# Performance work log

Hardware: AMD Instinct MI355X
Metric: run time of the kernel (lower is better)

The kernel has to match this reference:

```python
import jax, jax.numpy as jnp
import numpy as np

B = 16384      # batch
F = 26         # onehot fields
E = 32         # embedding_dim
L = 50         # multihot bag length
V = 1000000    # num_embeddings
CT = 13        # continuous features
D0, D1, D2, D3 = 909, 512, 256, 1
LEAKY = 0.01


def _leaky(x):
    return jnp.where(x >= 0, x, LEAKY * x)


def setup_inputs() -> dict:
    key = jax.random.key(0)
    ks = jax.random.split(key, 16)
    inp = {
        "onehot_i": jax.random.randint(ks[0], (B, F), 0, V),
        "onehot_x": jax.random.uniform(ks[1], (B, F), dtype=jnp.float32),
        "multihot_i1": jax.random.randint(ks[2], (B, L), 0, V),
        "multihot_x1": jax.random.uniform(ks[3], (B, L), dtype=jnp.float32),
        "multihot_i2": jax.random.randint(ks[4], (B, L), 0, V),
        "multihot_x2": jax.random.uniform(ks[5], (B, L), dtype=jnp.float32),
        "ctns": jax.random.normal(ks[6], (B, CT), dtype=jnp.float32),
        # learned parameters
        "wide_table": jax.random.normal(ks[7], (V, 1), dtype=jnp.float32) * 0.02,
        "deep_table": jax.random.normal(ks[8], (V, E), dtype=jnp.float32) * 0.02,
        "w2": jax.random.normal(ks[9], (D1, D0), dtype=jnp.float32) * (1.0 / np.sqrt(D0)),
        "b2": jnp.zeros((D1,), dtype=jnp.float32),
        "w3": jax.random.normal(ks[10], (D2, D1), dtype=jnp.float32) * (1.0 / np.sqrt(D1)),
        "b3": jnp.zeros((D2,), dtype=jnp.float32),
        "w4": jax.random.normal(ks[11], (D3, D2), dtype=jnp.float32) * (1.0 / np.sqrt(D2)),
        "b4": jnp.zeros((D3,), dtype=jnp.float32),
    }
    return inp


def reference(onehot_i, onehot_x, multihot_i1, multihot_x1, multihot_i2,
              multihot_x2, ctns, wide_table, deep_table, w2, b2, w3, b3, w4, b4):
    # ---- wide part ----
    # Original broadcasts the [B,F,1] wide embedding against x repeated E times,
    # then sums over all columns. That equals E * sum_f(w[idx]*x).
    wide_sum = (wide_table[onehot_i, 0] * onehot_x).sum(axis=1)          # [B]
    wide_sum = wide_sum + (wide_table[multihot_i1, 0] * multihot_x1).sum(axis=1)
    wide_sum = wide_sum + (wide_table[multihot_i2, 0] * multihot_x2).sum(axis=1)
    wide_out = E * wide_sum                                              # [B]

    # ---- deep part: gather, scale by field weight, pool multihot bags ----
    d_one = (deep_table[onehot_i] * onehot_x[:, :, None]).reshape(B, F * E)   # [B, F*E]
    d_m1 = (deep_table[multihot_i1] * multihot_x1[:, :, None]).sum(axis=1)    # [B, E]
    d_m2 = (deep_table[multihot_i2] * multihot_x2[:, :, None]).sum(axis=1)    # [B, E]
    x = jnp.concatenate([d_one, d_m1, d_m2, ctns], axis=1)                    # [B, D0]

    # dropout p=0.0 (deterministic reference)
    x = _leaky(x @ w2.T + b2)
    x = _leaky(x @ w3.T + b3)
    x = (x @ w4.T + b4).squeeze(-1)                                           # [B]
    return jax.nn.sigmoid(x + wide_out)
```

## Files before the change

### kernel.cpp

```cpp
#include <hip/hip_runtime.h>
#include <hip/hip_bf16.h>
#include <math.h>

#define B_   16384
#define F_   26
#define E_   32
#define L_   50
#define CT_  13
#define D0_  909
#define D0P  928
#define D1_  512
#define D2_  256

typedef __bf16 bf16x8 __attribute__((ext_vector_type(8)));
typedef float f32x4 __attribute__((ext_vector_type(4)));

__device__ inline float bf2f(unsigned short u) {
    union { unsigned int i; float f; } v; v.i = ((unsigned int)u) << 16; return v.f;
}
__device__ inline unsigned short f2b(float f) {
    union { __hip_bfloat16 h; unsigned short u; } v;
    v.h = __float2bfloat16(f);
    return v.u;
}

__device__ inline void gld_lds16(const void* g, void* l) {
    __builtin_amdgcn_global_load_lds(
        (const __attribute__((address_space(1))) unsigned int*)g,
        (__attribute__((address_space(3))) unsigned int*)l, 16, 0, 0);
}

#define W2N (D1_ * D0P)
#define W3N (D2_ * D1_)
__global__ __launch_bounds__(256) void cvt_weights(
    const float* __restrict__ w2, const float* __restrict__ w3,
    __hip_bfloat16* __restrict__ o2, __hip_bfloat16* __restrict__ o3)
{
    int i = blockIdx.x * 256 + threadIdx.x;
    if (i < W2N) {
        int r = i / D0P, c = i - r * D0P;
        float v = (c < D0_) ? w2[r * D0_ + c] : 0.f;
        o2[i] = __float2bfloat16(v);
    } else {
        int j = i - W2N;
        if (j < W3N) o3[j] = __float2bfloat16(w3[j]);
    }
}

__global__ __launch_bounds__(256) void embed_kernel(
    const int* __restrict__ oi, const float* __restrict__ ox,
    const int* __restrict__ i1, const float* __restrict__ x1,
    const int* __restrict__ i2, const float* __restrict__ x2,
    const float* __restrict__ ct, const float* __restrict__ wtab,
    const float* __restrict__ dtab,
    __hip_bfloat16* __restrict__ x0, float* __restrict__ wide)
{
    const int s    = blockIdx.x * 4 + (threadIdx.x >> 6);
    const int lane = threadIdx.x & 63;
    const int g    = lane >> 3;
    const int l    = lane & 7;
    __hip_bfloat16* xrow = x0 + (size_t)s * D0P;
    const float4* dt4 = (const float4*)dtab;

#pragma unroll
    for (int f0 = 0; f0 < 32; f0 += 8) {
        int f = f0 + g;
        if (f < F_) {
            int   idx = oi[s * F_ + f];
            float xv  = ox[s * F_ + f];
            float4 v  = dt4[(size_t)idx * 8 + l];
            ushort4 o;
            o.x = f2b(v.x * xv); o.y = f2b(v.y * xv);
            o.z = f2b(v.z * xv); o.w = f2b(v.w * xv);
            *(ushort4*)(xrow + f * E_ + l * 4) = o;
        }
    }

    float4 a1 = {0.f, 0.f, 0.f, 0.f}, a2 = {0.f, 0.f, 0.f, 0.f};
#pragma unroll
    for (int j0 = 0; j0 < 56; j0 += 8) {
        int j = j0 + g;
        if (j < L_) {
            int   k1 = i1[s * L_ + j];  float xv1 = x1[s * L_ + j];
            int   k2 = i2[s * L_ + j];  float xv2 = x2[s * L_ + j];
            float4 v1 = dt4[(size_t)k1 * 8 + l];
            float4 v2 = dt4[(size_t)k2 * 8 + l];
            a1.x = fmaf(v1.x, xv1, a1.x); a1.y = fmaf(v1.y, xv1, a1.y);
            a1.z = fmaf(v1.z, xv1, a1.z); a1.w = fmaf(v1.w, xv1, a1.w);
            a2.x = fmaf(v2.x, xv2, a2.x); a2.y = fmaf(v2.y, xv2, a2.y);
            a2.z = fmaf(v2.z, xv2, a2.z); a2.w = fmaf(v2.w, xv2, a2.w);
        }
    }
#pragma unroll
    for (int m = 8; m < 64; m <<= 1) {
        a1.x += __shfl_xor(a1.x, m); a1.y += __shfl_xor(a1.y, m);
        a1.z += __shfl_xor(a1.z, m); a1.w += __shfl_xor(a1.w, m);
        a2.x += __shfl_xor(a2.x, m); a2.y += __shfl_xor(a2.y, m);
        a2.z += __shfl_xor(a2.z, m); a2.w += __shfl_xor(a2.w, m);
    }
    if (g == 0) {
        ushort4 o;
        o.x = f2b(a1.x); o.y = f2b(a1.y); o.z = f2b(a1.z); o.w = f2b(a1.w);
        *(ushort4*)(xrow + F_ * E_ + l * 4) = o;
    }
    if (g == 1) {
        ushort4 o;
        o.x = f2b(a2.x); o.y = f2b(a2.y); o.z = f2b(a2.z); o.w = f2b(a2.w);
        *(ushort4*)(xrow + F_ * E_ + E_ + l * 4) = o;
    }
    if (lane < E_) {
        float v = (lane < CT_) ? ct[s * CT_ + lane] : 0.f;
        xrow[F_ * E_ + 2 * E_ + lane] = __float2bfloat16(v);
    }
    float acc = 0.f;
#pragma unroll
    for (int t = lane; t < F_ + 2 * L_; t += 64) {
        int idx; float xv;
        if (t < F_)            { idx = oi[s * F_ + t];            xv = ox[s * F_ + t]; }
        else if (t < F_ + L_)  { int j = t - F_;       idx = i1[s * L_ + j]; xv = x1[s * L_ + j]; }
        else                   { int j = t - F_ - L_;  idx = i2[s * L_ + j]; xv = x2[s * L_ + j]; }
        acc += wtab[idx] * xv;
    }
    for (int o = 32; o; o >>= 1) acc += __shfl_xor(acc, o);
    if (lane == 0) wide[s] = (float)E_ * acc;
}

template<int N, int K, bool ACT>
__global__ __launch_bounds__(256) void gemm_bias(
    const __hip_bfloat16* __restrict__ A,
    const __hip_bfloat16* __restrict__ W,
    const float* __restrict__ bias,
    __hip_bfloat16* __restrict__ C, int MBLKS)
{
    __shared__ __hip_bfloat16 As[128 * 32];
    __shared__ __hip_bfloat16 Bs[128 * 32];

    const int bm   = blockIdx.x % MBLKS;
    const int bn   = blockIdx.x / MBLKS;
    const int tid  = threadIdx.x;
    const int lane = tid & 63;
    const int w    = tid >> 6;
    const int wm   = w >> 1, wn = w & 1;

    f32x4 acc[4][4] = {};

    const int srow = lane >> 2;
    const int scol = (lane & 3) * 8;
    const __hip_bfloat16* Aw0 = A + ((size_t)bm * 128 + w * 32 + srow) * K + scol;
    const __hip_bfloat16* Aw1 = Aw0 + (size_t)16 * K;
    const __hip_bfloat16* Ww0 = W + ((size_t)bn * 128 + w * 32 + srow) * K + scol;
    const __hip_bfloat16* Ww1 = Ww0 + (size_t)16 * K;
    char* AsW = (char*)As + w * 2048;
    char* BsW = (char*)Bs + w * 2048;

    const int fr = lane & 15;
    const int kg = (lane >> 4) * 8;

    for (int k0 = 0; k0 < K; k0 += 32) {
        gld_lds16(Aw0 + k0, AsW);
        gld_lds16(Aw1 + k0, AsW + 1024);
        gld_lds16(Ww0 + k0, BsW);
        gld_lds16(Ww1 + k0, BsW + 1024);
        __syncthreads();

        bf16x8 af[4], bfv[4];
#pragma unroll
        for (int i = 0; i < 4; i++)
            af[i] = *(const bf16x8*)(As + (wm * 64 + i * 16 + fr) * 32 + kg);
#pragma unroll
        for (int i = 0; i < 4; i++)
            bfv[i] = *(const bf16x8*)(Bs + (wn * 64 + i * 16 + fr) * 32 + kg);
#pragma unroll
        for (int i = 0; i < 4; i++)
#pragma unroll
            for (int j = 0; j < 4; j++)
                acc[i][j] = __builtin_amdgcn_mfma_f32_16x16x32_bf16(af[i], bfv[j], acc[i][j], 0, 0, 0);
        __syncthreads();
    }

    float bv[4];
#pragma unroll
    for (int j = 0; j < 4; j++) bv[j] = bias[bn * 128 + wn * 64 + j * 16 + fr];
    const int crow0 = bm * 128 + wm * 64 + (lane >> 4) * 4;
    const int ccol0 = bn * 128 + wn * 64 + fr;
#pragma unroll
    for (int i = 0; i < 4; i++)
#pragma unroll
        for (int j = 0; j < 4; j++)
#pragma unroll
            for (int r = 0; r < 4; r++) {
                float v = acc[i][j][r] + bv[j];
                if (ACT) v = (v >= 0.f) ? v : 0.01f * v;
                C[(size_t)(crow0 + i * 16 + r) * N + ccol0 + j * 16] = __float2bfloat16(v);
            }
}

__global__ __launch_bounds__(256) void final_kernel(
    const __hip_bfloat16* __restrict__ h2, const float* __restrict__ w4,
    const float* __restrict__ b4, const float* __restrict__ wide,
    float* __restrict__ out)
{
    const int s    = blockIdx.x * 4 + (threadIdx.x >> 6);
    const int lane = threadIdx.x & 63;
    const unsigned short* hp = (const unsigned short*)(h2 + (size_t)s * D2_);
    ushort4 hv = *(const ushort4*)(hp + lane * 4);
    float4  wv = *(const float4*)(w4 + lane * 4);
    float acc = bf2f(hv.x) * wv.x + bf2f(hv.y) * wv.y + bf2f(hv.z) * wv.z + bf2f(hv.w) * wv.w;
    for (int o = 32; o; o >>= 1) acc += __shfl_xor(acc, o);
    if (lane == 0) {
        float x = acc + b4[0] + wide[s];
        out[s] = 1.f / (1.f + expf(-x));
    }
}

extern "C" void kernel_launch(void* const* d_in, const int* in_sizes, int n_in,
                              void* d_out, int out_size, void* d_ws, size_t ws_size,
                              hipStream_t stream) {
    const int*   oi  = (const int*)  d_in[0];
    const float* ox  = (const float*)d_in[1];
    const int*   i1  = (const int*)  d_in[2];
    const float* x1  = (const float*)d_in[3];
    const int*   i2  = (const int*)  d_in[4];
    const float* x2  = (const float*)d_in[5];
    const float* ct  = (const float*)d_in[6];
    const float* wt  = (const float*)d_in[7];
    const float* dt  = (const float*)d_in[8];
    const float* w2  = (const float*)d_in[9];
    const float* b2  = (const float*)d_in[10];
    const float* w3  = (const float*)d_in[11];
    const float* b3  = (const float*)d_in[12];
    const float* w4  = (const float*)d_in[13];
    const float* b4  = (const float*)d_in[14];
    float* out = (float*)d_out;

    char* ws = (char*)d_ws;
    __hip_bfloat16* x0b = (__hip_bfloat16*)(ws);
    __hip_bfloat16* h1b = (__hip_bfloat16*)(ws + 30408704);
    __hip_bfloat16* h2b = (__hip_bfloat16*)(ws + 47185920);
    float*          wid = (float*)         (ws + 55574528);
    __hip_bfloat16* w2b = (__hip_bfloat16*)(ws + 55640064);
    __hip_bfloat16* w3b = (__hip_bfloat16*)(ws + 56590336);

    cvt_weights<<<(W2N + W3N + 255) / 256, 256, 0, stream>>>(w2, w3, w2b, w3b);
    embed_kernel<<<4096, 256, 0, stream>>>(oi, ox, i1, x1, i2, x2, ct, wt, dt, x0b, wid);
    gemm_bias<D1_, D0P, true ><<<128 * (D1_ / 128), 256, 0, stream>>>(x0b, w2b, b2, h1b, 128);
    gemm_bias<D2_, D1_, true ><<<128 * (D2_ / 128), 256, 0, stream>>>(h1b, w3b, b3, h2b, 128);
    final_kernel<<<4096, 256, 0, stream>>>(h2b, w4, b4, wid, out);
}
```

Baseline: 126.5 us.

## Convert embedding table to bf16 before gathering and halve GEMM M-tile

Adds a kernel that converts the whole 1M x 32 fp32 deep table to bf16 in workspace on every call, then gathers from that bf16 copy, used only when the workspace is large enough. Separately, the GEMM tile is reduced from 128 to 64 rows so twice as many blocks launch. The table conversion streams 128MB in and writes 64MB per call to save on roughly 2M scattered 128B gathers, which is likely a net cost. The smaller M tile adds parallelism but reduces reuse of the weight tiles.

```diff
diff --git a/kernel.cpp b/kernel.cpp
--- a/kernel.cpp
+++ b/kernel.cpp
@@ -11,9 +11,12 @@
 #define D0P  928
 #define D1_  512
 #define D2_  256
+#define V_   1000000
+#define VE_  (V_ * E_)
 
 typedef __bf16 bf16x8 __attribute__((ext_vector_type(8)));
 typedef float f32x4 __attribute__((ext_vector_type(4)));
+typedef unsigned short u16x8 __attribute__((ext_vector_type(8)));
 
 __device__ inline float bf2f(unsigned short u) {
     union { unsigned int i; float f; } v; v.i = ((unsigned int)u) << 16; return v.f;
@@ -28,6 +31,19 @@
     __builtin_amdgcn_global_load_lds(
         (const __attribute__((address_space(1))) unsigned int*)g,
         (__attribute__((address_space(3))) unsigned int*)l, 16, 0, 0);
+}
+
+__global__ __launch_bounds__(256) void cvt_table(const float* __restrict__ dt,
+                                                 unsigned short* __restrict__ tb) {
+    size_t stride = (size_t)gridDim.x * 256 * 8;
+    for (size_t i = ((size_t)blockIdx.x * 256 + threadIdx.x) * 8; i < (size_t)VE_; i += stride) {
+        f32x4 a = __builtin_nontemporal_load((const f32x4*)(dt + i));
+        f32x4 b = __builtin_nontemporal_load((const f32x4*)(dt + i + 4));
+        u16x8 o;
+        o[0] = f2b(a.x); o[1] = f2b(a.y); o[2] = f2b(a.z); o[3] = f2b(a.w);
+        o[4] = f2b(b.x); o[5] = f2b(b.y); o[6] = f2b(b.z); o[7] = f2b(b.w);
+        *(u16x8*)(tb + i) = o;
+    }
 }
 
 #define W2N (D1_ * D0P)
@@ -47,7 +63,89 @@
     }
 }
 
-__global__ __launch_bounds__(256) void embed_kernel(
+__global__ __launch_bounds__(256) void embed_bf16(
+    const int* __restrict__ oi, const float* __restrict__ ox,
+    const int* __restrict__ i1, const float* __restrict__ x1,
+    const int* __restrict__ i2, const float* __restrict__ x2,
+    const float* __restrict__ ct, const float* __restrict__ wtab,
+    const unsigned short* __restrict__ tb,
+    __hip_bfloat16* __restrict__ x0, float* __restrict__ wide)
+{
+    const int s    = blockIdx.x * 4 + (threadIdx.x >> 6);
+    const int lane = threadIdx.x & 63;
+    const int g    = lane >> 2;
+    const int l    = lane & 3;
+    unsigned short* xrow = (unsigned short*)(x0 + (size_t)s * D0P);
+
+#pragma unroll
+    for (int f0 = 0; f0 < 32; f0 += 16) {
+        int f = f0 + g;
+        if (f < F_) {
+            int   idx = oi[s * F_ + f];
+            float xv  = ox[s * F_ + f];
+            u16x8 v = *(const u16x8*)(tb + (size_t)idx * E_ + l * 8);
+            u16x8 o;
+#pragma unroll
+            for (int e = 0; e < 8; e++) o[e] = f2b(bf2f(v[e]) * xv);
+            *(u16x8*)(xrow + f * E_ + l * 8) = o;
+        }
+    }
+
+    float a1[8] = {0.f,0.f,0.f,0.f,0.f,0.f,0.f,0.f};
+    float a2[8] = {0.f,0.f,0.f,0.f,0.f,0.f,0.f,0.f};
+#pragma unroll
+    for (int j0 = 0; j0 < 64; j0 += 16) {
+        int j = j0 + g;
+        if (j < L_) {
+            int   k1  = i1[s * L_ + j];  float xv1 = x1[s * L_ + j];
+            int   k2  = i2[s * L_ + j];  float xv2 = x2[s * L_ + j];
+            u16x8 v1 = *(const u16x8*)(tb + (size_t)k1 * E_ + l * 8);
+            u16x8 v2 = *(const u16x8*)(tb + (size_t)k2 * E_ + l * 8);
+#pragma unroll
+            for (int e = 0; e < 8; e++) {
+                a1[e] = fmaf(bf2f(v1[e]), xv1, a1[e]);
+                a2[e] = fmaf(bf2f(v2[e]), xv2, a2[e]);
+            }
+        }
+    }
+#pragma unroll
+    for (int m = 4; m < 64; m <<= 1) {
+#pragma unroll
+        for (int e = 0; e < 8; e++) {
+            a1[e] += __shfl_xor(a1[e], m);
+            a2[e] += __shfl_xor(a2[e], m);
+        }
+    }
+    if (g == 0) {
+        u16x8 o;
+#pragma unroll
+        for (int e = 0; e < 8; e++) o[e] = f2b(a1[e]);
+        *(u16x8*)(xrow + F_ * E_ + l * 8) = o;
+    }
+    if (g == 1) {
+        u16x8 o;
+#pragma unroll
+        for (int e = 0; e < 8; e++) o[e] = f2b(a2[e]);
+        *(u16x8*)(xrow + F_ * E_ + E_ + l * 8) = o;
+    }
+    if (lane < E_) {
+        float v = (lane < CT_) ? ct[s * CT_ + lane] : 0.f;
+        xrow[F_ * E_ + 2 * E_ + lane] = f2b(v);
+    }
+    float acc = 0.f;
+#pragma unroll
+    for (int t = lane; t < F_ + 2 * L_; t += 64) {
+        int idx; float xv;
+        if (t < F_)            { idx = oi[s * F_ + t];            xv = ox[s * F_ + t]; }
+        else if (t < F_ + L_)  { int j = t - F_;       idx = i1[s * L_ + j]; xv = x1[s * L_ + j]; }
+        else                   { int j = t - F_ - L_;  idx = i2[s * L_ + j]; xv = x2[s * L_ + j]; }
+        acc += wtab[idx] * xv;
+    }
+    for (int o = 32; o; o >>= 1) acc += __shfl_xor(acc, o);
+    if (lane == 0) wide[s] = (float)E_ * acc;
+}
+
+__global__ __launch_bounds__(256) void embed_fp32(
     const int* __restrict__ oi, const float* __restrict__ ox,
     const int* __restrict__ i1, const float* __restrict__ x1,
     const int* __restrict__ i2, const float* __restrict__ x2,
@@ -59,8 +157,8 @@
     const int lane = threadIdx.x & 63;
     const int g    = lane >> 3;
     const int l    = lane & 7;
-    __hip_bfloat16* xrow = x0 + (size_t)s * D0P;
-    const float4* dt4 = (const float4*)dtab;
+    unsigned short* xrow = (unsigned short*)(x0 + (size_t)s * D0P);
+    const f32x4* dt4 = (const f32x4*)dtab;
 
 #pragma unroll
     for (int f0 = 0; f0 < 32; f0 += 8) {
@@ -68,23 +166,22 @@
         if (f < F_) {
             int   idx = oi[s * F_ + f];
             float xv  = ox[s * F_ + f];
-            float4 v  = dt4[(size_t)idx * 8 + l];
+            f32x4 v   = dt4[(size_t)idx * 8 + l];
             ushort4 o;
             o.x = f2b(v.x * xv); o.y = f2b(v.y * xv);
             o.z = f2b(v.z * xv); o.w = f2b(v.w * xv);
             *(ushort4*)(xrow + f * E_ + l * 4) = o;
         }
     }
-
-    float4 a1 = {0.f, 0.f, 0.f, 0.f}, a2 = {0.f, 0.f, 0.f, 0.f};
+    f32x4 a1 = {0.f,0.f,0.f,0.f}, a2 = {0.f,0.f,0.f,0.f};
 #pragma unroll
     for (int j0 = 0; j0 < 56; j0 += 8) {
         int j = j0 + g;
         if (j < L_) {
-            int   k1 = i1[s * L_ + j];  float xv1 = x1[s * L_ + j];
-            int   k2 = i2[s * L_ + j];  float xv2 = x2[s * L_ + j];
-            float4 v1 = dt4[(size_t)k1 * 8 + l];
-            float4 v2 = dt4[(size_t)k2 * 8 + l];
+            int k1 = i1[s * L_ + j];  float xv1 = x1[s * L_ + j];
+            int k2 = i2[s * L_ + j];  float xv2 = x2[s * L_ + j];
+            f32x4 v1 = dt4[(size_t)k1 * 8 + l];
+            f32x4 v2 = dt4[(size_t)k2 * 8 + l];
             a1.x = fmaf(v1.x, xv1, a1.x); a1.y = fmaf(v1.y, xv1, a1.y);
             a1.z = fmaf(v1.z, xv1, a1.z); a1.w = fmaf(v1.w, xv1, a1.w);
             a2.x = fmaf(v2.x, xv2, a2.x); a2.y = fmaf(v2.y, xv2, a2.y);
@@ -99,18 +196,16 @@
         a2.z += __shfl_xor(a2.z, m); a2.w += __shfl_xor(a2.w, m);
     }
     if (g == 0) {
-        ushort4 o;
-        o.x = f2b(a1.x); o.y = f2b(a1.y); o.z = f2b(a1.z); o.w = f2b(a1.w);
+        ushort4 o; o.x = f2b(a1.x); o.y = f2b(a1.y); o.z = f2b(a1.z); o.w = f2b(a1.w);
         *(ushort4*)(xrow + F_ * E_ + l * 4) = o;
     }
     if (g == 1) {
-        ushort4 o;
-        o.x = f2b(a2.x); o.y = f2b(a2.y); o.z = f2b(a2.z); o.w = f2b(a2.w);
+        ushort4 o; o.x = f2b(a2.x); o.y = f2b(a2.y); o.z = f2b(a2.z); o.w = f2b(a2.w);
         *(ushort4*)(xrow + F_ * E_ + E_ + l * 4) = o;
     }
     if (lane < E_) {
         float v = (lane < CT_) ? ct[s * CT_ + lane] : 0.f;
-        xrow[F_ * E_ + 2 * E_ + lane] = __float2bfloat16(v);
+        xrow[F_ * E_ + 2 * E_ + lane] = f2b(v);
     }
     float acc = 0.f;
 #pragma unroll
@@ -132,7 +227,7 @@
     const float* __restrict__ bias,
     __hip_bfloat16* __restrict__ C, int MBLKS)
 {
-    __shared__ __hip_bfloat16 As[128 * 32];
+    __shared__ __hip_bfloat16 As[64 * 32];
     __shared__ __hip_bfloat16 Bs[128 * 32];
 
     const int bm   = blockIdx.x % MBLKS;
@@ -142,36 +237,34 @@
     const int w    = tid >> 6;
     const int wm   = w >> 1, wn = w & 1;
 
-    f32x4 acc[4][4] = {};
+    f32x4 acc[2][4] = {};
 
     const int srow = lane >> 2;
     const int scol = (lane & 3) * 8;
-    const __hip_bfloat16* Aw0 = A + ((size_t)bm * 128 + w * 32 + srow) * K + scol;
-    const __hip_bfloat16* Aw1 = Aw0 + (size_t)16 * K;
+    const __hip_bfloat16* Aw  = A + ((size_t)bm * 64  + w * 16 + srow) * K + scol;
     const __hip_bfloat16* Ww0 = W + ((size_t)bn * 128 + w * 32 + srow) * K + scol;
     const __hip_bfloat16* Ww1 = Ww0 + (size_t)16 * K;
-    char* AsW = (char*)As + w * 2048;
+    char* AsW = (char*)As + w * 1024;
     char* BsW = (char*)Bs + w * 2048;
 
     const int fr = lane & 15;
     const int kg = (lane >> 4) * 8;
 
     for (int k0 = 0; k0 < K; k0 += 32) {
-        gld_lds16(Aw0 + k0, AsW);
-        gld_lds16(Aw1 + k0, AsW + 1024);
+        gld_lds16(Aw  + k0, AsW);
         gld_lds16(Ww0 + k0, BsW);
         gld_lds16(Ww1 + k0, BsW + 1024);
         __syncthreads();
 
-        bf16x8 af[4], bfv[4];
-#pragma unroll
-        for (int i = 0; i < 4; i++)
-            af[i] = *(const bf16x8*)(As + (wm * 64 + i * 16 + fr) * 32 + kg);
-#pragma unroll
-        for (int i = 0; i < 4; i++)
-            bfv[i] = *(const bf16x8*)(Bs + (wn * 64 + i * 16 + fr) * 32 + kg);
-#pragma unroll
-        for (int i = 0; i < 4; i++)
+        bf16x8 af[2], bfv[4];
+#pragma unroll
+        for (int i = 0; i < 2; i++)
+            af[i] = *(const bf16x8*)(As + (wm * 32 + i * 16 + fr) * 32 + kg);
+#pragma unroll
+        for (int j = 0; j < 4; j++)
+            bfv[j] = *(const bf16x8*)(Bs + (wn * 64 + j * 16 + fr) * 32 + kg);
+#pragma unroll
+        for (int i = 0; i < 2; i++)
 #pragma unroll
             for (int j = 0; j < 4; j++)
                 acc[i][j] = __builtin_amdgcn_mfma_f32_16x16x32_bf16(af[i], bfv[j], acc[i][j], 0, 0, 0);
@@ -181,10 +274,10 @@
     float bv[4];
 #pragma unroll
     for (int j = 0; j < 4; j++) bv[j] = bias[bn * 128 + wn * 64 + j * 16 + fr];
-    const int crow0 = bm * 128 + wm * 64 + (lane >> 4) * 4;
+    const int crow0 = bm * 64 + wm * 32 + (lane >> 4) * 4;
     const int ccol0 = bn * 128 + wn * 64 + fr;
 #pragma unroll
-    for (int i = 0; i < 4; i++)
+    for (int i = 0; i < 2; i++)
 #pragma unroll
         for (int j = 0; j < 4; j++)
 #pragma unroll
@@ -233,17 +326,28 @@
     const float* b4  = (const float*)d_in[14];
     float* out = (float*)d_out;
 
+    const size_t TBBYTES = 64000000ULL;
+    const size_t NEED    = TBBYTES + 56852480ULL;
+    const bool   big     = ws_size >= NEED;
+
     char* ws = (char*)d_ws;
-    __hip_bfloat16* x0b = (__hip_bfloat16*)(ws);
-    __hip_bfloat16* h1b = (__hip_bfloat16*)(ws + 30408704);
-    __hip_bfloat16* h2b = (__hip_bfloat16*)(ws + 47185920);
-    float*          wid = (float*)         (ws + 55574528);
-    __hip_bfloat16* w2b = (__hip_bfloat16*)(ws + 55640064);
-    __hip_bfloat16* w3b = (__hip_bfloat16*)(ws + 56590336);
+    size_t off = big ? TBBYTES : 0;
+    unsigned short* tbl = (unsigned short*)ws;
+    __hip_bfloat16* x0b = (__hip_bfloat16*)(ws + off);
+    __hip_bfloat16* h1b = (__hip_bfloat16*)(ws + off + 30408704);
+    __hip_bfloat16* h2b = (__hip_bfloat16*)(ws + off + 47185920);
+    float*          wid = (float*)         (ws + off + 55574528);
+    __hip_bfloat16* w2b = (__hip_bfloat16*)(ws + off + 55640064);
+    __hip_bfloat16* w3b = (__hip_bfloat16*)(ws + off + 56590336);
 
     cvt_weights<<<(W2N + W3N + 255) / 256, 256, 0, stream>>>(w2, w3, w2b, w3b);
-    embed_kernel<<<4096, 256, 0, stream>>>(oi, ox, i1, x1, i2, x2, ct, wt, dt, x0b, wid);
-    gemm_bias<D1_, D0P, true ><<<128 * (D1_ / 128), 256, 0, stream>>>(x0b, w2b, b2, h1b, 128);
-    gemm_bias<D2_, D1_, true ><<<128 * (D2_ / 128), 256, 0, stream>>>(h1b, w3b, b3, h2b, 128);
+    if (big) {
+        cvt_table<<<4096, 256, 0, stream>>>(dt, tbl);
+        embed_bf16<<<4096, 256, 0, stream>>>(oi, ox, i1, x1, i2, x2, ct, wt, tbl, x0b, wid);
+    } else {
+        embed_fp32<<<4096, 256, 0, stream>>>(oi, ox, i1, x1, i2, x2, ct, wt, dt, x0b, wid);
+    }
+    gemm_bias<D1_, D0P, true ><<<256 * (D1_ / 128), 256, 0, stream>>>(x0b, w2b, b2, h1b, 256);
+    gemm_bias<D2_, D1_, true ><<<256 * (D2_ / 128), 256, 0, stream>>>(h1b, w3b, b3, h2b, 256);
     final_kernel<<<4096, 256, 0, stream>>>(h2b, w4, b4, wid, out);
 }
```

After: 152.4 us. 1.2x slower.
